# Performance work log

Hardware: AMD Instinct MI355X
Metric: run time of the kernel (lower is better)

Reference implementation:

```python
import jax, jax.numpy as jnp
import numpy as np


def setup_inputs() -> dict:
    key = jax.random.key(0)
    ks = jax.random.split(key, 12)
    B, S, D = 2, 1024, 1024       # batch, seq_len, hidden
    DF_S, DF_E, E = 2048, 512, 8   # shared ffn, expert ffn, n_experts
    W = 0.02                       # weight init scale
    x = jax.random.normal(ks[0], (B, S, D), jnp.float32)
    router_weight = jax.random.normal(ks[1], (E, D), jnp.float32) * W
    sh_gate_w = jax.random.normal(ks[2], (DF_S, D), jnp.float32) * W
    sh_up_w = jax.random.normal(ks[3], (DF_S, D), jnp.float32) * W
    sh_down_w = jax.random.normal(ks[4], (D, DF_S), jnp.float32) * W
    gate_q = jax.random.randint(ks[5], (E, DF_E, D), -128, 128, jnp.int32)
    up_q = jax.random.randint(ks[6], (E, DF_E, D), -128, 128, jnp.int32)
    down_q = jax.random.randint(ks[7], (E, D, DF_E), -128, 128, jnp.int32)
    gate_s = jax.random.uniform(ks[8], (E, DF_E), jnp.float32) * 0.001
    up_s = jax.random.uniform(ks[9], (E, DF_E), jnp.float32) * 0.001
    down_s = jax.random.uniform(ks[10], (E, D), jnp.float32) * 0.001
    alpha = 0.5 + jax.random.uniform(ks[11], (E,), jnp.float32)  # effective_alpha per expert
    return dict(x=x, router_weight=router_weight, sh_gate_w=sh_gate_w,
                sh_up_w=sh_up_w, sh_down_w=sh_down_w, gate_s=gate_s,
                up_s=up_s, down_s=down_s, alpha=alpha, gate_q=gate_q,
                up_q=up_q, down_q=down_q, top_k=2)


def reference(x, router_weight, sh_gate_w, sh_up_w, sh_down_w,
              gate_s, up_s, down_s, alpha, gate_q, up_q, down_q, top_k):
    B, S, D = x.shape
    T = B * S
    E = router_weight.shape[0]
    xf = x.reshape(T, D).astype(jnp.float32)
    # shared SwiGLU MLP
    shared = (jax.nn.silu(xf @ sh_gate_w.T) * (xf @ sh_up_w.T)) @ sh_down_w.T  # [T, D]
    # router: top-k + softmax over selected logits
    logits = xf @ router_weight.T                                # [T, E]
    k = min(int(top_k), E)
    vals, idx = jax.lax.top_k(logits, k)
    w = jax.nn.softmax(vals, axis=-1)                            # [T, k]
    # scatter routing weights into dense combine matrix [T, E] (topk idx are distinct)
    combine = jnp.zeros((T, E), jnp.float32).at[jnp.arange(T)[:, None], idx].add(w)
    # on-the-fly dequantization: int8-range quants * per-row scale
    gw = gate_q.astype(jnp.float32) * gate_s[..., None]          # [E, DF_E, D]
    uw = up_q.astype(jnp.float32) * up_s[..., None]              # [E, DF_E, D]
    dw = down_q.astype(jnp.float32) * down_s[..., None]          # [E, D, DF_E]
    # expert SwiGLU for every (token, expert) pair, combined by routing weights
    g = jnp.einsum('td,efd->tef', xf, gw)                        # [T, E, DF_E]
    u = jnp.einsum('td,efd->tef', xf, uw)
    eo = jnp.einsum('tef,edf->ted', jax.nn.silu(g) * u, dw)      # [T, E, D]
    delta = eo - shared[:, None, :]                              # expert output minus shared
    mixed = shared + jnp.einsum('te,ted->td', combine * alpha[None, :], delta)
    return mixed.reshape(B, S, D)
```

## Files before the change

kernel.cpp:

```cpp
#include <hip/hip_runtime.h>
#include <math.h>

#define T_TOK 2048
#define D_DIM 1024
#define E_NUM 8
#define DFS   2048
#define DFE   512

#define BK 32

typedef short short8 __attribute__((ext_vector_type(8)));
typedef float floatx4 __attribute__((ext_vector_type(4)));
typedef unsigned short ushort;

__device__ __forceinline__ ushort f2b(float f) {
  union { float f; unsigned u; } v; v.f = f;
  unsigned r = (v.u + 0x7fffu + ((v.u >> 16) & 1u)) >> 16;
  return (ushort)r;
}

__device__ __forceinline__ void gld16(const ushort* g, ushort* l) {
  __builtin_amdgcn_global_load_lds(
      (const __attribute__((address_space(1))) void*)g,
      (__attribute__((address_space(3))) void*)l,
      16, 0, 0);
}

__device__ __forceinline__ float silu_mul(float g, float u) {
  return (g / (1.f + __expf(-g))) * u;
}

__global__ __launch_bounds__(256) void mega_prep(
    const float* __restrict__ x, const float* __restrict__ rw,
    const float* __restrict__ alpha,
    const float* __restrict__ sg, const float* __restrict__ su,
    const float* __restrict__ sd,
    const int* __restrict__ gq, const int* __restrict__ uq,
    const int* __restrict__ dq,
    int* __restrict__ choice, float2* __restrict__ cpair,
    float* __restrict__ csum, ushort* __restrict__ xb,
    ushort* __restrict__ sgb, ushort* __restrict__ subb,
    ushort* __restrict__ sdb,
    ushort* __restrict__ gqb, ushort* __restrict__ uqb,
    ushort* __restrict__ dqb) {
  const int b = blockIdx.x;
  const int tid = threadIdx.x;
  if (b < 512) {
    __shared__ float xs[4 * D_DIM];
    const size_t base = (size_t)b * 4 * D_DIM;
#pragma unroll
    for (int j = 0; j < 4; ++j) {
      const int idx = j * 1024 + tid * 4;
      float4 v = *(const float4*)(x + base + idx);
      *(float4*)&xs[idx] = v;
      union { ushort u[4]; uint2 p; } o;
      o.u[0] = f2b(v.x); o.u[1] = f2b(v.y); o.u[2] = f2b(v.z); o.u[3] = f2b(v.w);
      *(uint2*)(xb + base + idx) = o.p;
    }
    __syncthreads();
    const int w = tid >> 6, l = tid & 63;
    const int t = b * 4 + w;
    const int e = l >> 3, sub = l & 7;
    const float* wr = rw + e * D_DIM;
    float acc = 0.f;
#pragma unroll
    for (int k = 0; k < 32; ++k) {
      const int d = k * 32 + sub * 4;
      float4 xv = *(const float4*)&xs[w * D_DIM + d];
      float4 wv = *(const float4*)(wr + d);
      acc += xv.x * wv.x + xv.y * wv.y + xv.z * wv.z + xv.w * wv.w;
    }
    acc += __shfl_xor(acc, 1);
    acc += __shfl_xor(acc, 2);
    acc += __shfl_xor(acc, 4);
    float lg[8];
#pragma unroll
    for (int i = 0; i < 8; ++i) lg[i] = __shfl(acc, i * 8);
    if (l == 0) {
      int i0 = 0; float v0 = lg[0];
#pragma unroll
      for (int i = 1; i < E_NUM; ++i) if (lg[i] > v0) { v0 = lg[i]; i0 = i; }
      int i1 = -1; float v1 = -1e30f;
#pragma unroll
      for (int i = 0; i < E_NUM; ++i) {
        if (i == i0) continue;
        if (lg[i] > v1) { v1 = lg[i]; i1 = i; }
      }
      float w0 = 1.f / (1.f + __expf(v1 - v0));
      float w1 = 1.f - w0;
      float c0 = w0 * alpha[i0];
      float c1 = w1 * alpha[i1];
      csum[t] = c0 + c1;
      choice[t] = i0 | (i1 << 4);
      cpair[t] = make_float2(c0, c1);
    }
  } else if (b < 512 + 3072) {
    const int bb = b - 512;
    const int which = bb >> 10;
    const float* src; ushort* dst;
    if (which == 0) { src = sg; dst = sgb; }
    else if (which == 1) { src = su; dst = subb; }
    else { src = sd; dst = sdb; }
    const size_t i = (size_t)(bb & 1023) * 256 + tid;
    const float4* sp = (const float4*)src;
    float4 a = sp[2 * i], c = sp[2 * i + 1];
    union { ushort u[8]; uint4 v; } o;
    o.u[0] = f2b(a.x); o.u[1] = f2b(a.y); o.u[2] = f2b(a.z); o.u[3] = f2b(a.w);
    o.u[4] = f2b(c.x); o.u[5] = f2b(c.y); o.u[6] = f2b(c.z); o.u[7] = f2b(c.w);
    ((uint4*)dst)[i] = o.v;
  } else {
    const int bb = b - 3584;
    const int which = bb >> 11;
    const int* src; ushort* dst;
    if (which == 0) { src = gq; dst = gqb; }
    else if (which == 1) { src = uq; dst = uqb; }
    else { src = dq; dst = dqb; }
    const size_t i = (size_t)(bb & 2047) * 256 + tid;
    const int4* sp = (const int4*)src;
    int4 a = sp[2 * i], c = sp[2 * i + 1];
    union { ushort u[8]; uint4 v; } o;
    o.u[0] = f2b((float)a.x); o.u[1] = f2b((float)a.y);
    o.u[2] = f2b((float)a.z); o.u[3] = f2b((float)a.w);
    o.u[4] = f2b((float)c.x); o.u[5] = f2b((float)c.y);
    o.u[6] = f2b((float)c.z); o.u[7] = f2b((float)c.w);
    ((uint4*)dst)[i] = o.v;
  }
}

__global__ __launch_bounds__(1024) void build_lists(
    const int* __restrict__ choice, int* __restrict__ cnt,
    int* __restrict__ tok_list, uint2* __restrict__ ass) {
  __shared__ int lcnt[E_NUM];
  __shared__ int lbase[E_NUM];
  const int tid = threadIdx.x;
  if (tid < E_NUM) lcnt[tid] = 0;
  __syncthreads();
  uint2 tmp[T_TOK / 1024];
#pragma unroll
  for (int r = 0; r < T_TOK / 1024; ++r) {
    const int t = r * 1024 + tid;
    const int ch = choice[t];
    const int i0 = ch & 15, i1 = ch >> 4;
    const int p0 = atomicAdd(&lcnt[i0], 1);
    tok_list[i0 * T_TOK + p0] = t;
    const int p1 = atomicAdd(&lcnt[i1], 1);
    tok_list[i1 * T_TOK + p1] = t;
    tmp[r] = make_uint2((unsigned)((i0 << 16) | p0), (unsigned)((i1 << 16) | p1));
  }
  __syncthreads();
  if (tid < E_NUM) {
    int b = 0;
    for (int i = 0; i < tid; ++i) b += lcnt[i];
    lbase[tid] = b;
    cnt[tid] = lcnt[tid];
    cnt[8 + tid] = b;
  }
  __syncthreads();
#pragma unroll
  for (int r = 0; r < T_TOK / 1024; ++r) {
    const int t = r * 1024 + tid;
    const uint2 v = tmp[r];
    ass[t] = make_uint2(lbase[v.x >> 16] + (v.x & 0xffffu),
                        lbase[v.y >> 16] + (v.y & 0xffffu));
  }
}

__global__ __launch_bounds__(256) void mfma_gateup_all(
    const ushort* __restrict__ xb,
    const ushort* __restrict__ wg, const ushort* __restrict__ wu,
    const ushort* __restrict__ gq, const ushort* __restrict__ uq,
    const float* __restrict__ gate_s, const float* __restrict__ up_s,
    const int* __restrict__ cnt, const int* __restrict__ tok_list,
    ushort* __restrict__ sbuf, ushort* __restrict__ act) {
  const int bid = blockIdx.x;
  const bool is_sh = (bid < 512);
  const int tid = threadIdx.x;
  const int wave = tid >> 6, lane = tid & 63;
  const int wr = wave >> 1, wc = wave & 1;
  const int srow = lane >> 2;
  const int scol = (lane & 3) * 8;
  const int K = D_DIM;

  int m0, n0, e = 0, ce = 0, ebase = 0;
  const ushort *aR0, *aR1, *g0, *u0;
  if (is_sh) {
    n0 = (bid & 31) * 64;
    m0 = (bid >> 5) * 128;
    aR0 = xb + (size_t)(m0 + wave * 16 + srow) * K + scol;
    aR1 = aR0 + (size_t)64 * K;
    g0 = wg + (size_t)(n0 + wave * 16 + srow) * K + scol;
    u0 = wu + (size_t)(n0 + wave * 16 + srow) * K + scol;
  } else {
    const int r = bid - 512;
    e = r >> 7;
    const int rr = r & 127;
    n0 = (rr & 7) * 64;
    m0 = (rr >> 3) * 128;
    ce = cnt[e];
    if (m0 >= ce) return;
    ebase = cnt[8 + e];
    const int r0 = m0 + wave * 16 + srow;
    const int r1 = r0 + 64;
    const int tk0 = (r0 < ce) ? tok_list[e * T_TOK + r0] : 0;
    const int tk1 = (r1 < ce) ? tok_list[e * T_TOK + r1] : 0;
    aR0 = xb + (size_t)tk0 * K + scol;
    aR1 = xb + (size_t)tk1 * K + scol;
    g0 = gq + (size_t)e * DFE * D_DIM + (size_t)(n0 + wave * 16 + srow) * K + scol;
    u0 = uq + (size_t)e * DFE * D_DIM + (size_t)(n0 + wave * 16 + srow) * K + scol;
  }

  __shared__ ushort As[2 * 128 * BK];
  __shared__ ushort Bg[2 * 64 * BK];
  __shared__ ushort Bu[2 * 64 * BK];
  ushort* lA = &As[(wave * 16) * BK];
  ushort* lG = &Bg[(wave * 16) * BK];
  ushort* lU = &Bu[(wave * 16) * BK];

  floatx4 accg[4][2], accu[4][2];
#pragma unroll
  for (int i = 0; i < 4; ++i)
#pragma unroll
    for (int j = 0; j < 2; ++j) { accg[i][j] = (floatx4)(0.f); accu[i][j] = (floatx4)(0.f); }

  const int kc = (lane >> 4) * 8;
  const int rb = lane & 15;

#define STAGE_GU(bu, ks)                                   \
  do {                                                     \
    gld16(aR0 + (ks), lA + (bu) * 128 * BK);               \
    gld16(aR1 + (ks), lA + (bu) * 128 * BK + 64 * BK);     \
    gld16(g0 + (ks), lG + (bu) * 64 * BK);                 \
    gld16(u0 + (ks), lU + (bu) * 64 * BK);                 \
  } while (0)

  const int NK = K / BK;
  STAGE_GU(0, 0);
  __syncthreads();

  for (int k = 0; k < NK; ++k) {
    const int cur = k & 1;
    if (k + 1 < NK) STAGE_GU(cur ^ 1, (k + 1) * BK);
    const int boA = cur * 128 * BK;
    const int boB = cur * 64 * BK;
    short8 af[4], gf[2], uf[2];
#pragma unroll
    for (int mt = 0; mt < 4; ++mt)
      af[mt] = *(const short8*)&As[boA + (wr * 64 + mt * 16 + rb) * BK + kc];
#pragma unroll
    for (int nt = 0; nt < 2; ++nt) {
      gf[nt] = *(const short8*)&Bg[boB + (wc * 32 + nt * 16 + rb) * BK + kc];
      uf[nt] = *(const short8*)&Bu[boB + (wc * 32 + nt * 16 + rb) * BK + kc];
    }
#pragma unroll
    for (int mt = 0; mt < 4; ++mt)
#pragma unroll
      for (int nt = 0; nt < 2; ++nt) {
        accg[mt][nt] = __builtin_amdgcn_mfma_f32_16x16x32_bf16(af[mt], gf[nt], accg[mt][nt], 0, 0, 0);
        accu[mt][nt] = __builtin_amdgcn_mfma_f32_16x16x32_bf16(af[mt], uf[nt], accu[mt][nt], 0, 0, 0);
      }
    __syncthreads();
  }
#undef STAGE_GU

  if (is_sh) {
#pragma unroll
    for (int mt = 0; mt < 4; ++mt)
#pragma unroll
      for (int nt = 0; nt < 2; ++nt) {
        const int col = n0 + wc * 32 + nt * 16 + rb;
#pragma unroll
        for (int r = 0; r < 4; ++r) {
          const int row = m0 + wr * 64 + mt * 16 + (lane >> 4) * 4 + r;
          float s = silu_mul(accg[mt][nt][r], accu[mt][nt][r]);
          sbuf[(size_t)row * DFS + col] = f2b(s);
        }
      }
  } else {
#pragma unroll
    for (int mt = 0; mt < 4; ++mt)
#pragma unroll
      for (int nt = 0; nt < 2; ++nt) {
        const int col = n0 + wc * 32 + nt * 16 + rb;
        const float gsc = gate_s[e * DFE + col];
        const float usc = up_s[e * DFE + col];
#pragma unroll
        for (int r = 0; r < 4; ++r) {
          const int slot = m0 + wr * 64 + mt * 16 + (lane >> 4) * 4 + r;
          if (slot < ce) {
            float s = silu_mul(accg[mt][nt][r] * gsc, accu[mt][nt][r] * usc);
            act[(size_t)(ebase + slot) * DFE + col] = f2b(s);
          }
        }
      }
  }
}

__global__ __launch_bounds__(256) void mfma_down_all(
    const ushort* __restrict__ sb, const ushort* __restrict__ wd,
    const ushort* __restrict__ act, const ushort* __restrict__ dq,
    const float* __restrict__ down_s, const int* __restrict__ cnt,
    float* __restrict__ shd0, float* __restrict__ shd1,
    float* __restrict__ pbuf) {
  const int bid = blockIdx.x;
  const bool is_sh = (bid < 256);
  const int tid = threadIdx.x;
  const int wave = tid >> 6, lane = tid & 63;
  const int wr = wave >> 1, wc = wave & 1;
  const int srow = lane >> 2;
  const int scol = (lane & 3) * 8;

  int m0, n0, e = 0, ce = 0, ebase = 0, klen;
  const ushort *aR0, *aR1, *bR0, *bR1;
  float* dst;
  if (is_sh) {
    const int z = bid >> 7;
    const int rr = bid & 127;
    n0 = (rr & 7) * 128;
    m0 = (rr >> 3) * 128;
    const int kb = z * (DFS / 2);
    klen = DFS / 2;
    dst = z ? shd1 : shd0;
    aR0 = sb + (size_t)(m0 + wave * 16 + srow) * DFS + kb + scol;
    aR1 = aR0 + (size_t)64 * DFS;
    bR0 = wd + (size_t)(n0 + wave * 16 + srow) * DFS + kb + scol;
    bR1 = bR0 + (size_t)64 * DFS;
  } else {
    const int r = bid - 256;
    e = r >> 7;
    const int rr = r & 127;
    n0 = (rr & 7) * 128;
    m0 = (rr >> 3) * 128;
    ce = cnt[e];
    if (m0 >= ce) return;
    ebase = cnt[8 + e];
    klen = DFE;
    dst = pbuf;
    aR0 = act + (size_t)(ebase + m0 + wave * 16 + srow) * DFE + scol;
    aR1 = aR0 + (size_t)64 * DFE;
    bR0 = dq + (size_t)e * D_DIM * DFE + (size_t)(n0 + wave * 16 + srow) * DFE + scol;
    bR1 = bR0 + (size_t)64 * DFE;
  }

  __shared__ ushort As[2 * 128 * BK];
  __shared__ ushort Bs[2 * 128 * BK];
  ushort* lA = &As[(wave * 16) * BK];
  ushort* lB = &Bs[(wave * 16) * BK];

  floatx4 acc[4][4];
#pragma unroll
  for (int i = 0; i < 4; ++i)
#pragma unroll
    for (int j = 0; j < 4; ++j) acc[i][j] = (floatx4)(0.f);

  const int kc = (lane >> 4) * 8;
  const int rb = lane & 15;

#define STAGE_DN(bu, ks)                                   \
  do {                                                     \
    gld16(aR0 + (ks), lA + (bu) * 128 * BK);               \
    gld16(aR1 + (ks), lA + (bu) * 128 * BK + 64 * BK);     \
    gld16(bR0 + (ks), lB + (bu) * 128 * BK);               \
    gld16(bR1 + (ks), lB + (bu) * 128 * BK + 64 * BK);     \
  } while (0)

  const int NK = klen / BK;
  STAGE_DN(0, 0);
  __syncthreads();

  for (int k = 0; k < NK; ++k) {
    const int cur = k & 1;
    if (k + 1 < NK) STAGE_DN(cur ^ 1, (k + 1) * BK);
    const int bo = cur * 128 * BK;
    short8 af[4], bf[4];
#pragma unroll
    for (int mt = 0; mt < 4; ++mt)
      af[mt] = *(const short8*)&As[bo + (wr * 64 + mt * 16 + rb) * BK + kc];
#pragma unroll
    for (int nt = 0; nt < 4; ++nt)
      bf[nt] = *(const short8*)&Bs[bo + (wc * 64 + nt * 16 + rb) * BK + kc];
#pragma unroll
    for (int mt = 0; mt < 4; ++mt)
#pragma unroll
      for (int nt = 0; nt < 4; ++nt)
        acc[mt][nt] = __builtin_amdgcn_mfma_f32_16x16x32_bf16(af[mt], bf[nt], acc[mt][nt], 0, 0, 0);
    __syncthreads();
  }
#undef STAGE_DN

  if (is_sh) {
#pragma unroll
    for (int mt = 0; mt < 4; ++mt)
#pragma unroll
      for (int nt = 0; nt < 4; ++nt) {
        const int col = n0 + wc * 64 + nt * 16 + rb;
#pragma unroll
        for (int r = 0; r < 4; ++r) {
          const int row = m0 + wr * 64 + mt * 16 + (lane >> 4) * 4 + r;
          dst[(size_t)row * D_DIM + col] = acc[mt][nt][r];
        }
      }
  } else {
#pragma unroll
    for (int mt = 0; mt < 4; ++mt)
#pragma unroll
      for (int nt = 0; nt < 4; ++nt) {
        const int col = n0 + wc * 64 + nt * 16 + rb;
        const float dsc = down_s[e * D_DIM + col];
#pragma unroll
        for (int r = 0; r < 4; ++r) {
          const int slot = m0 + wr * 64 + mt * 16 + (lane >> 4) * 4 + r;
          if (slot < ce)
            dst[(size_t)(ebase + slot) * D_DIM + col] = acc[mt][nt][r] * dsc;
        }
      }
  }
}

__global__ __launch_bounds__(256) void combine_kernel(
    const float* __restrict__ shd0, const float* __restrict__ shd1,
    const float* __restrict__ pbuf, const float* __restrict__ csum,
    const float2* __restrict__ cpair, const uint2* __restrict__ ass,
    float* __restrict__ out) {
  const int t = blockIdx.x;
  const int c4 = threadIdx.x * 4;
  const float cs = 1.f - csum[t];
  const float2 cp = cpair[t];
  const uint2 a = ass[t];
  const size_t idx = (size_t)t * D_DIM + c4;
  float4 s0 = *(const float4*)(shd0 + idx);
  float4 s1 = *(const float4*)(shd1 + idx);
  float4 e0 = *(const float4*)(pbuf + (size_t)a.x * D_DIM + c4);
  float4 e1 = *(const float4*)(pbuf + (size_t)a.y * D_DIM + c4);
  float4 o;
  o.x = cs * (s0.x + s1.x) + cp.x * e0.x + cp.y * e1.x;
  o.y = cs * (s0.y + s1.y) + cp.x * e0.y + cp.y * e1.y;
  o.z = cs * (s0.z + s1.z) + cp.x * e0.z + cp.y * e1.z;
  o.w = cs * (s0.w + s1.w) + cp.x * e0.w + cp.y * e1.w;
  *(float4*)(out + idx) = o;
}

extern "C" void kernel_launch(void* const* d_in, const int* in_sizes, int n_in,
                              void* d_out, int out_size, void* d_ws, size_t ws_size,
                              hipStream_t stream) {
  const float* x         = (const float*)d_in[0];
  const float* rw        = (const float*)d_in[1];
  const float* sh_gate_w = (const float*)d_in[2];
  const float* sh_up_w   = (const float*)d_in[3];
  const float* sh_down_w = (const float*)d_in[4];
  const float* gate_s    = (const float*)d_in[5];
  const float* up_s      = (const float*)d_in[6];
  const float* down_s    = (const float*)d_in[7];
  const float* alpha     = (const float*)d_in[8];
  const int*   gate_q    = (const int*)d_in[9];
  const int*   up_q      = (const int*)d_in[10];
  const int*   down_q    = (const int*)d_in[11];

  char* ws = (char*)d_ws;
  const size_t MB = 1u << 20;
  int*    cnt      = (int*)ws;
  int*    tok_list = (int*)(ws + 1024);
  float*  csum     = (float*)(ws + 66560);
  int*    choice   = (int*)(ws + 74752);
  float2* cpair    = (float2*)(ws + 82944);
  uint2*  ass      = (uint2*)(ws + 99328);
  ushort* xb      = (ushort*)(ws + 1 * MB);
  ushort* sgb     = (ushort*)(ws + 5 * MB);
  ushort* sub     = (ushort*)(ws + 9 * MB);
  float*  shd0    = (float*)(ws + 5 * MB);
  ushort* sbuf    = (ushort*)(ws + 13 * MB);
  ushort* sdb     = (ushort*)(ws + 21 * MB);
  ushort* gqb     = (ushort*)(ws + 25 * MB);
  ushort* uqb     = (ushort*)(ws + 33 * MB);
  float*  pbuf    = (float*)(ws + 25 * MB);
  ushort* dqb     = (ushort*)(ws + 41 * MB);
  ushort* act     = (ushort*)(ws + 49 * MB);
  float*  shd1    = (float*)(ws + 53 * MB);

  float* out = (float*)d_out;

  mega_prep<<<9728, 256, 0, stream>>>(
      x, rw, alpha, sh_gate_w, sh_up_w, sh_down_w, gate_q, up_q, down_q,
      choice, cpair, csum, xb, sgb, sub, sdb, gqb, uqb, dqb);
  build_lists<<<1, 1024, 0, stream>>>(choice, cnt, tok_list, ass);

  mfma_gateup_all<<<512 + 1024, 256, 0, stream>>>(
      xb, sgb, sub, gqb, uqb, gate_s, up_s, cnt, tok_list, sbuf, act);
  mfma_down_all<<<256 + 1024, 256, 0, stream>>>(
      sbuf, sdb, act, dqb, down_s, cnt, shd0, shd1, pbuf);
  combine_kernel<<<T_TOK, 256, 0, stream>>>(shd0, shd1, pbuf, csum, cpair, ass, out);
}
```

Measured before the change: 232.2 us.

## Triple-buffer LDS staging with explicit vmcnt waits and one barrier per K step

Both MoE GEMM kernels (gate/up and down) move from double-buffered to triple-buffered LDS, with A and B tiles merged into one ring of three stages. Global-to-LDS loads are issued two stages ahead and completed with explicit s_waitcnt vmcnt counts, which leaves a single barrier per iteration instead of one before and one after compute. The aim is to hide more global-load latency behind the MFMA work and cut synchronisation overhead. The cost is 50% more shared memory per block, which may reduce occupancy, and correctness now depends on hand-written waitcnt counts and on the stage-reuse ordering being right.

```diff
diff --git a/kernel.cpp b/kernel.cpp
--- a/kernel.cpp
+++ b/kernel.cpp
@@ -165,6 +165,8 @@
   }
 }
 
+#define SZGU (256 * BK)
+
 __global__ __launch_bounds__(256) void mfma_gateup_all(
     const ushort* __restrict__ xb,
     const ushort* __restrict__ wg, const ushort* __restrict__ wu,
@@ -209,12 +211,8 @@
     u0 = uq + (size_t)e * DFE * D_DIM + (size_t)(n0 + wave * 16 + srow) * K + scol;
   }
 
-  __shared__ ushort As[2 * 128 * BK];
-  __shared__ ushort Bg[2 * 64 * BK];
-  __shared__ ushort Bu[2 * 64 * BK];
-  ushort* lA = &As[(wave * 16) * BK];
-  ushort* lG = &Bg[(wave * 16) * BK];
-  ushort* lU = &Bu[(wave * 16) * BK];
+  __shared__ ushort L[3 * SZGU];
+  const int woff = (wave * 16) * BK;
 
   floatx4 accg[4][2], accu[4][2];
 #pragma unroll
@@ -225,32 +223,42 @@
   const int kc = (lane >> 4) * 8;
   const int rb = lane & 15;
 
-#define STAGE_GU(bu, ks)                                   \
-  do {                                                     \
-    gld16(aR0 + (ks), lA + (bu) * 128 * BK);               \
-    gld16(aR1 + (ks), lA + (bu) * 128 * BK + 64 * BK);     \
-    gld16(g0 + (ks), lG + (bu) * 64 * BK);                 \
-    gld16(u0 + (ks), lU + (bu) * 64 * BK);                 \
+  ushort* s0 = L;
+  ushort* s1 = L + SZGU;
+  ushort* s2 = L + 2 * SZGU;
+
+#define STAGE_GU(bs)                                   \
+  do {                                                 \
+    gld16(aR0, (bs) + woff);                           \
+    gld16(aR1, (bs) + 64 * BK + woff);                 \
+    gld16(g0, (bs) + 128 * BK + woff);                 \
+    gld16(u0, (bs) + 192 * BK + woff);                 \
+    aR0 += BK; aR1 += BK; g0 += BK; u0 += BK;          \
   } while (0)
 
   const int NK = K / BK;
-  STAGE_GU(0, 0);
-  __syncthreads();
+  STAGE_GU(s0);
+  STAGE_GU(s1);
 
   for (int k = 0; k < NK; ++k) {
-    const int cur = k & 1;
-    if (k + 1 < NK) STAGE_GU(cur ^ 1, (k + 1) * BK);
-    const int boA = cur * 128 * BK;
-    const int boB = cur * 64 * BK;
+    if (k < NK - 1) {
+      asm volatile("s_waitcnt vmcnt(4)" ::: "memory");
+    } else {
+      asm volatile("s_waitcnt vmcnt(0)" ::: "memory");
+    }
+    __builtin_amdgcn_s_barrier();
     short8 af[4], gf[2], uf[2];
 #pragma unroll
     for (int mt = 0; mt < 4; ++mt)
-      af[mt] = *(const short8*)&As[boA + (wr * 64 + mt * 16 + rb) * BK + kc];
+      af[mt] = *(const short8*)&s0[(wr * 64 + mt * 16 + rb) * BK + kc];
 #pragma unroll
     for (int nt = 0; nt < 2; ++nt) {
-      gf[nt] = *(const short8*)&Bg[boB + (wc * 32 + nt * 16 + rb) * BK + kc];
-      uf[nt] = *(const short8*)&Bu[boB + (wc * 32 + nt * 16 + rb) * BK + kc];
+      gf[nt] = *(const short8*)&s0[128 * BK + (wc * 32 + nt * 16 + rb) * BK + kc];
+      uf[nt] = *(const short8*)&s0[192 * BK + (wc * 32 + nt * 16 + rb) * BK + kc];
     }
+    if (k + 2 < NK) STAGE_GU(s2);
+    asm volatile("s_waitcnt lgkmcnt(0)" ::: "memory");
+    __builtin_amdgcn_sched_barrier(0);
 #pragma unroll
     for (int mt = 0; mt < 4; ++mt)
 #pragma unroll
@@ -258,7 +266,7 @@
         accg[mt][nt] = __builtin_amdgcn_mfma_f32_16x16x32_bf16(af[mt], gf[nt], accg[mt][nt], 0, 0, 0);
         accu[mt][nt] = __builtin_amdgcn_mfma_f32_16x16x32_bf16(af[mt], uf[nt], accu[mt][nt], 0, 0, 0);
       }
-    __syncthreads();
+    ushort* t = s0; s0 = s1; s1 = s2; s2 = t;
   }
 #undef STAGE_GU
 
@@ -294,6 +302,8 @@
       }
   }
 }
+
+#define SZDN (256 * BK)
 
 __global__ __launch_bounds__(256) void mfma_down_all(
     const ushort* __restrict__ sb, const ushort* __restrict__ wd,
@@ -341,10 +351,8 @@
     bR1 = bR0 + (size_t)64 * DFE;
   }
 
-  __shared__ ushort As[2 * 128 * BK];
-  __shared__ ushort Bs[2 * 128 * BK];
-  ushort* lA = &As[(wave * 16) * BK];
-  ushort* lB = &Bs[(wave * 16) * BK];
+  __shared__ ushort L[3 * SZDN];
+  const int woff = (wave * 16) * BK;
 
   floatx4 acc[4][4];
 #pragma unroll
@@ -355,35 +363,46 @@
   const int kc = (lane >> 4) * 8;
   const int rb = lane & 15;
 
-#define STAGE_DN(bu, ks)                                   \
-  do {                                                     \
-    gld16(aR0 + (ks), lA + (bu) * 128 * BK);               \
-    gld16(aR1 + (ks), lA + (bu) * 128 * BK + 64 * BK);     \
-    gld16(bR0 + (ks), lB + (bu) * 128 * BK);               \
-    gld16(bR1 + (ks), lB + (bu) * 128 * BK + 64 * BK);     \
+  ushort* s0 = L;
+  ushort* s1 = L + SZDN;
+  ushort* s2 = L + 2 * SZDN;
+
+#define STAGE_DN(bs)                                   \
+  do {                                                 \
+    gld16(aR0, (bs) + woff);                           \
+    gld16(aR1, (bs) + 64 * BK + woff);                 \
+    gld16(bR0, (bs) + 128 * BK + woff);                \
+    gld16(bR1, (bs) + 192 * BK + woff);                \
+    aR0 += BK; aR1 += BK; bR0 += BK; bR1 += BK;        \
   } while (0)
 
   const int NK = klen / BK;
-  STAGE_DN(0, 0);
-  __syncthreads();
+  STAGE_DN(s0);
+  STAGE_DN(s1);
 
   for (int k = 0; k < NK; ++k) {
-    const int cur = k & 1;
-    if (k + 1 < NK) STAGE_DN(cur ^ 1, (k + 1) * BK);
-    const int bo = cur * 128 * BK;
+    if (k < NK - 1) {
+      asm volatile("s_waitcnt vmcnt(4)" ::: "memory");
+    } else {
+      asm volatile("s_waitcnt vmcnt(0)" ::: "memory");
+    }
+    __builtin_amdgcn_s_barrier();
     short8 af[4], bf[4];
 #pragma unroll
     for (int mt = 0; mt < 4; ++mt)
-      af[mt] = *(const short8*)&As[bo + (wr * 64 + mt * 16 + rb) * BK + kc];
+      af[mt] = *(const short8*)&s0[(wr * 64 + mt * 16 + rb) * BK + kc];
 #pragma unroll
     for (int nt = 0; nt < 4; ++nt)
-      bf[nt] = *(const short8*)&Bs[bo + (wc * 64 + nt * 16 + rb) * BK + kc];
+      bf[nt] = *(const short8*)&s0[128 * BK + (wc * 64 + nt * 16 + rb) * BK + kc];
+    if (k + 2 < NK) STAGE_DN(s2);
+    asm volatile("s_waitcnt lgkmcnt(0)" ::: "memory");
+    __builtin_amdgcn_sched_barrier(0);
 #pragma unroll
     for (int mt = 0; mt < 4; ++mt)
 #pragma unroll
       for (int nt = 0; nt < 4; ++nt)
         acc[mt][nt] = __builtin_amdgcn_mfma_f32_16x16x32_bf16(af[mt], bf[nt], acc[mt][nt], 0, 0, 0);
-    __syncthreads();
+    ushort* t = s0; s0 = s1; s1 = s2; s2 = t;
   }
 #undef STAGE_DN
 
```

After: 225.0 us. 3.1% less time.
